# Performance work log

Measured on AMD Instinct MI355X. Metric: run time of the kernel, lower is better.

## Reference

```python
import jax, jax.numpy as jnp
import numpy as np

NUM_GRAPHS = 8
N_NODES = 50000
N_EDGES = 800000
F_IN = 128
HID = 256
EPS_BN = 1e-5


def _gat(x, ei, W, a_src, a_dst, b, heads, out_dim):
    # PyG GATConv: h = x @ W -> [N, heads, out]; edge (j=src -> i=dst)
    N = x.shape[0]
    h = (x @ W).reshape(N, heads, out_dim)
    alpha_src = jnp.sum(h * a_src, axis=-1)  # [N, H]
    alpha_dst = jnp.sum(h * a_dst, axis=-1)  # [N, H]
    src, dst = ei[0], ei[1]
    e = jax.nn.leaky_relu(alpha_src[src] + alpha_dst[dst], 0.2)  # [E, H]
    # segment softmax over edges grouped by destination node
    m = jax.ops.segment_max(e, dst, num_segments=N)
    m = jnp.where(jnp.isfinite(m), m, 0.0)
    ex = jnp.exp(e - m[dst])
    denom = jax.ops.segment_sum(ex, dst, num_segments=N)
    alpha = ex / (denom[dst] + 1e-16)
    msg = h[src] * alpha[:, :, None]  # [E, H, out]
    agg = jax.ops.segment_sum(msg, dst, num_segments=N)
    return agg.reshape(N, heads * out_dim) + b


def _bn(h, gamma, beta):
    # BatchNorm over nodes (training-mode batch statistics, biased variance)
    mu = h.mean(axis=0)
    var = h.var(axis=0)
    return gamma * (h - mu) / jnp.sqrt(var + EPS_BN) + beta


def setup_inputs() -> dict:
    key = jax.random.key(0)
    ks = jax.random.split(key, 16)
    s = 0.05
    inp = {
        "x": jax.random.normal(ks[0], (N_NODES, F_IN), dtype=jnp.float32),
        "edge_index": jax.random.randint(ks[1], (2, N_EDGES), 0, N_NODES, dtype=jnp.int64) if False else jax.random.randint(ks[1], (2, N_EDGES), 0, N_NODES),
        "batch_index": jnp.sort(jax.random.randint(ks[2], (N_NODES,), 0, NUM_GRAPHS)),
        # conv1: GATConv(128, 64, heads=4)
        "W1": jax.random.normal(ks[3], (F_IN, HID), dtype=jnp.float32) * s,
        "a_src1": jax.random.normal(ks[4], (4, 64), dtype=jnp.float32) * s,
        "a_dst1": jax.random.normal(ks[5], (4, 64), dtype=jnp.float32) * s,
        "b1": jnp.zeros((HID,), jnp.float32),
        "g1": jnp.ones((HID,), jnp.float32),
        "beta1": jnp.zeros((HID,), jnp.float32),
        # conv2: GATConv(256, 256, heads=1)
        "W2": jax.random.normal(ks[6], (HID, HID), dtype=jnp.float32) * s,
        "a_src2": jax.random.normal(ks[7], (1, HID), dtype=jnp.float32) * s,
        "a_dst2": jax.random.normal(ks[8], (1, HID), dtype=jnp.float32) * s,
        "b2": jnp.zeros((HID,), jnp.float32),
        "g2": jnp.ones((HID,), jnp.float32),
        "beta2": jnp.zeros((HID,), jnp.float32),
        # q_head: Linear(512,256) -> ReLU -> Linear(256,4)
        "Wq1": jax.random.normal(ks[9], (2 * HID, HID), dtype=jnp.float32) * s,
        "bq1": jnp.zeros((HID,), jnp.float32),
        "Wq2": jax.random.normal(ks[10], (HID, 4), dtype=jnp.float32) * s,
        "bq2": jnp.zeros((4,), jnp.float32),
    }
    return inp


def reference(x, edge_index, batch_index, W1, a_src1, a_dst1, b1, g1, beta1,
              W2, a_src2, a_dst2, b2, g2, beta2, Wq1, bq1, Wq2, bq2):
    N = x.shape[0]
    loops = jnp.arange(N, dtype=edge_index.dtype)
    ei = jnp.concatenate([edge_index, jnp.stack([loops, loops])], axis=1)
    h = jax.nn.relu(_bn(_gat(x, ei, W1, a_src1, a_dst1, b1, 4, 64), g1, beta1))
    h = jax.nn.relu(_bn(_gat(h, ei, W2, a_src2, a_dst2, b2, 1, HID), g2, beta2))
    sums = jax.ops.segment_sum(h, batch_index, num_segments=NUM_GRAPHS)
    cnt = jax.ops.segment_sum(jnp.ones((N, 1), h.dtype), batch_index, num_segments=NUM_GRAPHS)
    gmean = sums / jnp.maximum(cnt, 1.0)
    ctx = jnp.concatenate([h, gmean[batch_index]], axis=1)  # [N, 512]
    q = jax.nn.relu(ctx @ Wq1 + bq1) @ Wq2 + bq2  # [N, 4]
    return (q, batch_index)
```

## Files before the change

### kernel.cpp

```cpp
#include <hip/hip_runtime.h>
#include <hip/hip_bf16.h>
#include <math.h>

#define F_IN  128
#define HIDC  256
#define NG    8
#define EPS_BN 1e-5f

typedef unsigned short u16;
typedef unsigned int   u32;
typedef unsigned char  u8;
typedef __attribute__((ext_vector_type(8))) short bf16x8;
typedef __attribute__((ext_vector_type(4))) float f32x4;
typedef __attribute__((ext_vector_type(2))) float f32x2;

static __device__ __forceinline__ float b2f(u16 u) {
    return __uint_as_float((u32)u << 16);
}
static __device__ __forceinline__ u16 f2b(float f) {
    u32 u = __float_as_uint(f);
    u32 r = (u + 0x7fffu + ((u >> 16) & 1u)) >> 16;
    return (u16)r;
}
static __device__ __forceinline__ u32 pack2(float a, float b) {
    return (u32)f2b(a) | ((u32)f2b(b) << 16);
}
static __device__ __forceinline__ float lk(float v) {
    return v >= 0.f ? v : 0.2f * v;
}
static __device__ __forceinline__ u8 f2fp8(float v) {
    return (u8)__builtin_amdgcn_cvt_pk_fp8_f32(v, v, 0, false);
}

static __device__ __forceinline__ u16 frag_elem(const float* __restrict__ W,
                                                int i, int K) {
    int j = i & 7;
    int lane = (i >> 3) & 63;
    int rest = i >> 9;
    int ksteps = K >> 5;
    int kst = rest % ksteps;
    int ntile = rest / ksteps;
    int k = kst * 32 + (lane >> 4) * 8 + j;
    int n = ntile * 16 + (lane & 15);
    return f2b(W[(long)k * HIDC + n]);
}

__global__ void prep_kernel(const float* __restrict__ x,
                            const float* __restrict__ W1,
                            const float* __restrict__ W2,
                            const float* __restrict__ Wq1,
                            u32* __restrict__ xb, u16* __restrict__ WT1,
                            u16* __restrict__ WT2, u16* __restrict__ WQT,
                            int npair) {
    int i = blockIdx.x * 256 + threadIdx.x;
    if (i < npair) {
        float2 v = ((const float2*)x)[i];
        xb[i] = pack2(v.x, v.y);
        return;
    }
    i -= npair;
    if (i < F_IN * HIDC) { WT1[i] = frag_elem(W1, i, F_IN); return; }
    i -= F_IN * HIDC;
    if (i < HIDC * HIDC) { WT2[i] = frag_elem(W2, i, HIDC); return; }
    i -= HIDC * HIDC;
    if (i < HIDC * HIDC) { WQT[i] = frag_elem(Wq1, i, HIDC); }
}

__global__ void out_init_kernel(float* __restrict__ out,
                                const float* __restrict__ bq2,
                                const int* __restrict__ batch, int N) {
    int i = blockIdx.x * 256 + threadIdx.x;
    if (i < N * 4) out[i] = bq2[i & 3];
    else if (i < N * 5) out[i] = (float)batch[i - N * 4];
}

__global__ void bn_coef_kernel(const float* __restrict__ sum,
                               const float* __restrict__ sumsq,
                               const float* __restrict__ gamma,
                               const float* __restrict__ beta,
                               float* __restrict__ scale,
                               float* __restrict__ bias, int N) {
    int c = threadIdx.x;
    float invN = 1.f / (float)N;
    float mu = sum[c] * invN;
    float var = sumsq[c] * invN - mu * mu;
    float inv = rsqrtf(var + EPS_BN);
    float sc = gamma[c] * inv;
    scale[c] = sc;
    bias[c] = beta[c] - mu * sc;
}

template <int K, int MODE>
__global__ __launch_bounds__(256)
void gemm_mfma_kernel(const u16* __restrict__ A, const u16* __restrict__ WTf,
                      u8* __restrict__ C, int M,
                      const float* __restrict__ scaleA, const float* __restrict__ biasA,
                      const float* __restrict__ wsrc, const float* __restrict__ wdst,
                      float* __restrict__ asrc, float* __restrict__ adst,
                      const float* __restrict__ gproj, const int* __restrict__ bat,
                      const float* __restrict__ bq1,
                      const float* __restrict__ wq2, float* __restrict__ qout) {
    constexpr int KSTEPS = K / 32;
    constexpr int RCH = K / 8;
    __shared__ u16 sA[32][K + 8];
    int tid = threadIdx.x;
    int m0 = blockIdx.x * 32;

    for (int i = tid; i < 32 * RCH; i += 256) {
        int r = i / RCH, c = i % RCH;
        int gm = m0 + r;
        gm = gm < M ? gm : M - 1;
        *(uint4*)&sA[r][c * 8] = *(const uint4*)(A + (size_t)gm * K + c * 8);
    }
    __syncthreads();

    int wid = tid >> 6, lane = tid & 63;
    int row = lane & 15, quad = lane >> 4;
    int mf0 = m0, mf1 = m0 + 16;
    bool v1 = mf1 < M;

    f32x4 acc[2][4];
#pragma unroll
    for (int f = 0; f < 2; ++f)
#pragma unroll
        for (int t = 0; t < 4; ++t) acc[f][t] = (f32x4){0.f, 0.f, 0.f, 0.f};

    const u16* Bbase = WTf + ((size_t)(wid * 4) * KSTEPS * 64 + lane) * 8;

#pragma unroll
    for (int ks = 0; ks < KSTEPS; ++ks) {
        int kk = ks * 32 + quad * 8;
        bf16x8 a[2];
        a[0] = *(const bf16x8*)&sA[row][kk];
        a[1] = *(const bf16x8*)&sA[16 + row][kk];
        if constexpr (MODE != 0) {
            int c0 = kk;
            float4 s0 = *(const float4*)(scaleA + c0);
            float4 s1 = *(const float4*)(scaleA + c0 + 4);
            float4 b0 = *(const float4*)(biasA + c0);
            float4 b1 = *(const float4*)(biasA + c0 + 4);
#pragma unroll
            for (int f = 0; f < 2; ++f) {
                float xv[8];
#pragma unroll
                for (int j = 0; j < 8; ++j) xv[j] = b2f((u16)a[f][j]);
                xv[0] = fmaxf(fmaf(s0.x, xv[0], b0.x), 0.f);
                xv[1] = fmaxf(fmaf(s0.y, xv[1], b0.y), 0.f);
                xv[2] = fmaxf(fmaf(s0.z, xv[2], b0.z), 0.f);
                xv[3] = fmaxf(fmaf(s0.w, xv[3], b0.w), 0.f);
                xv[4] = fmaxf(fmaf(s1.x, xv[4], b1.x), 0.f);
                xv[5] = fmaxf(fmaf(s1.y, xv[5], b1.y), 0.f);
                xv[6] = fmaxf(fmaf(s1.z, xv[6], b1.z), 0.f);
                xv[7] = fmaxf(fmaf(s1.w, xv[7], b1.w), 0.f);
#pragma unroll
                for (int j = 0; j < 8; ++j) a[f][j] = (short)f2b(xv[j]);
            }
        }
#pragma unroll
        for (int t = 0; t < 4; ++t) {
            bf16x8 b = *(const bf16x8*)(Bbase + ((size_t)t * KSTEPS + ks) * 512);
            acc[0][t] = __builtin_amdgcn_mfma_f32_16x16x32_bf16(a[0], b, acc[0][t], 0, 0, 0);
            acc[1][t] = __builtin_amdgcn_mfma_f32_16x16x32_bf16(a[1], b, acc[1][t], 0, 0, 0);
        }
    }

    int n0 = wid * 64;
    int mf[2] = {mf0, mf1};
    bool vf[2] = {true, v1};
    if constexpr (MODE == 2) {
        float qacc[2][4][4];
#pragma unroll
        for (int f = 0; f < 2; ++f)
#pragma unroll
            for (int r = 0; r < 4; ++r)
#pragma unroll
                for (int j = 0; j < 4; ++j) qacc[f][r][j] = 0.f;
#pragma unroll
        for (int f = 0; f < 2; ++f) {
            if (!vf[f]) continue;
            int bm[4];
#pragma unroll
            for (int r = 0; r < 4; ++r) bm[r] = bat[mf[f] + quad * 4 + r];
#pragma unroll
            for (int t = 0; t < 4; ++t) {
                int n = n0 + t * 16 + row;
                float bq = bq1[n];
                float4 w4 = ((const float4*)wq2)[n];
#pragma unroll
                for (int r = 0; r < 4; ++r) {
                    float v = fmaxf(acc[f][t][r] + gproj[bm[r] * HIDC + n] + bq, 0.f);
                    qacc[f][r][0] = fmaf(v, w4.x, qacc[f][r][0]);
                    qacc[f][r][1] = fmaf(v, w4.y, qacc[f][r][1]);
                    qacc[f][r][2] = fmaf(v, w4.z, qacc[f][r][2]);
                    qacc[f][r][3] = fmaf(v, w4.w, qacc[f][r][3]);
                }
            }
        }
#pragma unroll
        for (int off = 1; off < 16; off <<= 1)
#pragma unroll
            for (int f = 0; f < 2; ++f)
#pragma unroll
                for (int r = 0; r < 4; ++r)
#pragma unroll
                    for (int j = 0; j < 4; ++j)
                        qacc[f][r][j] += __shfl_xor(qacc[f][r][j], off, 64);
        if (row == 0) {
#pragma unroll
            for (int f = 0; f < 2; ++f) {
                if (!vf[f]) continue;
#pragma unroll
                for (int r = 0; r < 4; ++r) {
                    size_t m = mf[f] + quad * 4 + r;
#pragma unroll
                    for (int j = 0; j < 4; ++j)
                        atomicAdd(&qout[m * 4 + j], qacc[f][r][j]);
                }
            }
        }
    } else {
#pragma unroll
        for (int f = 0; f < 2; ++f) {
            if (!vf[f]) continue;
#pragma unroll
            for (int t = 0; t < 4; ++t) {
                int n = n0 + t * 16 + row;
#pragma unroll
                for (int r = 0; r < 4; ++r)
                    C[(size_t)(mf[f] + quad * 4 + r) * HIDC + n] = f2fp8(acc[f][t][r]);
            }
        }
        if constexpr (MODE == 0) {
            float pa[2][4] = {}, pd[2][4] = {};
#pragma unroll
            for (int t = 0; t < 4; ++t) {
                float ws = wsrc[n0 + t * 16 + row];
                float wd = wdst[n0 + t * 16 + row];
#pragma unroll
                for (int f = 0; f < 2; ++f)
#pragma unroll
                    for (int r = 0; r < 4; ++r) {
                        pa[f][r] = fmaf(acc[f][t][r], ws, pa[f][r]);
                        pd[f][r] = fmaf(acc[f][t][r], wd, pd[f][r]);
                    }
            }
#pragma unroll
            for (int off = 1; off < 16; off <<= 1)
#pragma unroll
                for (int f = 0; f < 2; ++f)
#pragma unroll
                    for (int r = 0; r < 4; ++r) {
                        pa[f][r] += __shfl_xor(pa[f][r], off, 64);
                        pd[f][r] += __shfl_xor(pd[f][r], off, 64);
                    }
            if (row == 0) {
#pragma unroll
                for (int f = 0; f < 2; ++f) {
                    if (!vf[f]) continue;
#pragma unroll
                    for (int r = 0; r < 4; ++r) {
                        int m = mf[f] + quad * 4 + r;
                        asrc[m * 4 + wid] = pa[f][r];
                        adst[m * 4 + wid] = pd[f][r];
                    }
                }
            }
        }
        if constexpr (MODE == 1) {
            float pa[2][4] = {}, pd[2][4] = {};
#pragma unroll
            for (int t = 0; t < 4; ++t) {
                float ws = wsrc[n0 + t * 16 + row];
                float wd = wdst[n0 + t * 16 + row];
#pragma unroll
                for (int f = 0; f < 2; ++f)
#pragma unroll
                    for (int r = 0; r < 4; ++r) {
                        pa[f][r] = fmaf(acc[f][t][r], ws, pa[f][r]);
                        pd[f][r] = fmaf(acc[f][t][r], wd, pd[f][r]);
                    }
            }
#pragma unroll
            for (int off = 1; off < 16; off <<= 1)
#pragma unroll
                for (int f = 0; f < 2; ++f)
#pragma unroll
                    for (int r = 0; r < 4; ++r) {
                        pa[f][r] += __shfl_xor(pa[f][r], off, 64);
                        pd[f][r] += __shfl_xor(pd[f][r], off, 64);
                    }
            if (row == 0) {
#pragma unroll
                for (int f = 0; f < 2; ++f) {
                    if (!vf[f]) continue;
#pragma unroll
                    for (int r = 0; r < 4; ++r) {
                        int m = mf[f] + quad * 4 + r;
                        atomicAdd(&asrc[m], pa[f][r]);
                        atomicAdd(&adst[m], pd[f][r]);
                    }
                }
            }
        }
    }
}

__global__ void deg_kernel(const int* __restrict__ ei, int E, int N,
                           int* __restrict__ deg) {
    int e = blockIdx.x * blockDim.x + threadIdx.x;
    if (e >= E + N) return;
    int d = (e < E) ? ei[E + e] : (e - E);
    atomicAdd(&deg[d], 1);
}

__global__ __launch_bounds__(256)
void scan_phase1(const int* __restrict__ deg, int* __restrict__ part,
                 int* __restrict__ bsum, int N) {
    __shared__ int tmp[256];
    int i = blockIdx.x * 256 + threadIdx.x;
    int v = (i < N) ? deg[i] : 0;
    tmp[threadIdx.x] = v;
    __syncthreads();
    for (int off = 1; off < 256; off <<= 1) {
        int t = (threadIdx.x >= off) ? tmp[threadIdx.x - off] : 0;
        __syncthreads();
        tmp[threadIdx.x] += t;
        __syncthreads();
    }
    if (i < N) part[i] = tmp[threadIdx.x];
    if (threadIdx.x == 255) bsum[blockIdx.x] = tmp[255];
}
__global__ __launch_bounds__(256)
void scan_phase2(int* __restrict__ bsum, int nb) {
    __shared__ int tmp[256];
    int v = (threadIdx.x < nb) ? bsum[threadIdx.x] : 0;
    tmp[threadIdx.x] = v;
    __syncthreads();
    for (int off = 1; off < 256; off <<= 1) {
        int t = (threadIdx.x >= off) ? tmp[threadIdx.x - off] : 0;
        __syncthreads();
        tmp[threadIdx.x] += t;
        __syncthreads();
    }
    if (threadIdx.x < nb)
        bsum[threadIdx.x] = threadIdx.x ? tmp[threadIdx.x - 1] : 0;
}
__global__ __launch_bounds__(256)
void scan_phase3(const int* __restrict__ part, const int* __restrict__ bsum,
                 int* __restrict__ rowptr, int N) {
    int i = blockIdx.x * 256 + threadIdx.x;
    if (i < N) rowptr[i + 1] = part[i] + bsum[blockIdx.x];
    if (i == 0) rowptr[0] = 0;
}

__global__ void fill_kernel(const int* __restrict__ ei, int E, int N,
                            const int* __restrict__ rowptr,
                            int* __restrict__ cur, int* __restrict__ csr_src) {
    int e = blockIdx.x * blockDim.x + threadIdx.x;
    if (e >= E + N) return;
    int s = (e < E) ? ei[e] : (e - E);
    int d = (e < E) ? ei[E + e] : (e - E);
    int pos = rowptr[d] + atomicAdd(&cur[d], 1);
    csr_src[pos] = s;
}

template <int H>
__global__ __launch_bounds__(256)
void gat_gather_kernel(const int* __restrict__ rowptr,
                       const int* __restrict__ csr_src,
                       const float* __restrict__ asrc,
                       const float* __restrict__ adst,
                       const u8* __restrict__ h,
                       u16* __restrict__ agg, int N) {
    __shared__ __align__(16) uint2 s_ed[4][64 * H];
    int wid = threadIdx.x >> 6, lane = threadIdx.x & 63;
    int n = blockIdx.x * 4 + wid;
    if (n >= N) return;
    int start = rowptr[n], end = rowptr[n + 1];
    int deg = end - start;
    float ad[H];
#pragma unroll
    for (int hh = 0; hh < H; ++hh) ad[hh] = adst[n * H + hh];

    f32x2 acc01 = {0.f, 0.f}, acc23 = {0.f, 0.f};
    const int head = (H == 4) ? (lane >> 4) : 0;
    const u8* hb = h;
    const u32 laneB = (u32)lane * 4u;
    float wsum[H];

#define GBODY(J) {                                                             \
            uint2 e_ = s_ed[wid][(H == 4) ? ((J) * 4 + head) : (J)];           \
            u32 hv_ = *(const u32*)(hb + (size_t)(e_.x + laneB));              \
            float al_ = __uint_as_float(e_.y);                                 \
            f32x2 al2_ = {al_, al_};                                           \
            f32x2 v01_ = __builtin_amdgcn_cvt_pk_f32_fp8(hv_, false);          \
            f32x2 v23_ = __builtin_amdgcn_cvt_pk_f32_fp8(hv_, true);           \
            acc01 = __builtin_elementwise_fma(v01_, al2_, acc01);              \
            acc23 = __builtin_elementwise_fma(v23_, al2_, acc23); }

    if (deg <= 64) {
        float v[H];
#pragma unroll
        for (int hh = 0; hh < H; ++hh) v[hh] = -1e30f;
        u32 off = 0;
        if (lane < deg) {
            int s = csr_src[start + lane];
            off = (u32)s * (u32)HIDC;
            if (H == 4) {
                float4 a4 = *(const float4*)(asrc + s * 4);
                v[0] = lk(a4.x + ad[0]);
                v[1 % H] = lk(a4.y + ad[1 % H]);
                v[2 % H] = lk(a4.z + ad[2 % H]);
                v[3 % H] = lk(a4.w + ad[3 % H]);
            } else {
                v[0] = lk(asrc[s] + ad[0]);
            }
        }
        float m[H];
#pragma unroll
        for (int hh = 0; hh < H; ++hh) m[hh] = v[hh];
#pragma unroll
        for (int o = 1; o < 64; o <<= 1)
#pragma unroll
            for (int hh = 0; hh < H; ++hh)
                m[hh] = fmaxf(m[hh], __shfl_xor(m[hh], o, 64));
        float w[H];
#pragma unroll
        for (int hh = 0; hh < H; ++hh) {
            w[hh] = __expf(v[hh] - m[hh]);
            wsum[hh] = w[hh];
        }
#pragma unroll
        for (int o = 1; o < 64; o <<= 1)
#pragma unroll
            for (int hh = 0; hh < H; ++hh)
                wsum[hh] += __shfl_xor(wsum[hh], o, 64);
        if (H == 4) {
            uint4 w0, w1;
            w0.x = off; w0.y = __float_as_uint(w[0]);
            w0.z = off; w0.w = __float_as_uint(w[1 % H]);
            w1.x = off; w1.y = __float_as_uint(w[2 % H]);
            w1.z = off; w1.w = __float_as_uint(w[3 % H]);
            *(uint4*)&s_ed[wid][lane * 4] = w0;
            *(uint4*)&s_ed[wid][lane * 4 + 2] = w1;
        } else {
            s_ed[wid][lane] = make_uint2(off, __float_as_uint(w[0]));
        }
        int j = 0;
        for (; j + 4 <= deg; j += 4) { GBODY(j) GBODY(j + 1) GBODY(j + 2) GBODY(j + 3) }
        for (; j < deg; ++j) GBODY(j)
    } else {
        float m[H];
#pragma unroll
        for (int hh = 0; hh < H; ++hh) m[hh] = -1e30f;
        for (int i = start + lane; i < end; i += 64) {
            int s = csr_src[i];
            if (H == 4) {
                float4 a4 = *(const float4*)(asrc + s * 4);
                m[0] = fmaxf(m[0], lk(a4.x + ad[0]));
                m[1 % H] = fmaxf(m[1 % H], lk(a4.y + ad[1 % H]));
                m[2 % H] = fmaxf(m[2 % H], lk(a4.z + ad[2 % H]));
                m[3 % H] = fmaxf(m[3 % H], lk(a4.w + ad[3 % H]));
            } else {
                m[0] = fmaxf(m[0], lk(asrc[s] + ad[0]));
            }
        }
#pragma unroll
        for (int o = 1; o < 64; o <<= 1)
#pragma unroll
            for (int hh = 0; hh < H; ++hh)
                m[hh] = fmaxf(m[hh], __shfl_xor(m[hh], o, 64));
#pragma unroll
        for (int hh = 0; hh < H; ++hh) wsum[hh] = 0.f;
        for (int base = start; base < end; base += 64) {
            int cnt = min(64, end - base);
            if (lane < cnt) {
                int s = csr_src[base + lane];
                u32 off = (u32)s * (u32)HIDC;
                if (H == 4) {
                    float4 a4 = *(const float4*)(asrc + s * 4);
                    float w0f = __expf(lk(a4.x + ad[0]) - m[0]);
                    float w1f = __expf(lk(a4.y + ad[1 % H]) - m[1 % H]);
                    float w2f = __expf(lk(a4.z + ad[2 % H]) - m[2 % H]);
                    float w3f = __expf(lk(a4.w + ad[3 % H]) - m[3 % H]);
                    wsum[0] += w0f; wsum[1 % H] += w1f;
                    wsum[2 % H] += w2f; wsum[3 % H] += w3f;
                    uint4 w0, w1;
                    w0.x = off; w0.y = __float_as_uint(w0f);
                    w0.z = off; w0.w = __float_as_uint(w1f);
                    w1.x = off; w1.y = __float_as_uint(w2f);
                    w1.z = off; w1.w = __float_as_uint(w3f);
                    *(uint4*)&s_ed[wid][lane * 4] = w0;
                    *(uint4*)&s_ed[wid][lane * 4 + 2] = w1;
                } else {
                    float wf = __expf(lk(asrc[s] + ad[0]) - m[0]);
                    wsum[0] += wf;
                    s_ed[wid][lane] = make_uint2(off, __float_as_uint(wf));
                }
            }
            int j = 0;
            for (; j + 4 <= cnt; j += 4) { GBODY(j) GBODY(j + 1) GBODY(j + 2) GBODY(j + 3) }
            for (; j < cnt; ++j) GBODY(j)
        }
#pragma unroll
        for (int o = 1; o < 64; o <<= 1)
#pragma unroll
            for (int hh = 0; hh < H; ++hh)
                wsum[hh] += __shfl_xor(wsum[hh], o, 64);
    }
#undef GBODY
    float sc = 1.f / (wsum[head] + 1e-16f);
    f32x2 sc2 = {sc, sc};
    acc01 *= sc2;
    acc23 *= sc2;
    uint2 o;
    o.x = pack2(acc01.x, acc01.y);
    o.y = pack2(acc23.x, acc23.y);
    ((uint2*)(agg + (size_t)n * HIDC))[lane] = o;
}

__global__ __launch_bounds__(256)
void bn_stats_kernel(const u16* __restrict__ h, int N,
                     float* __restrict__ sum, float* __restrict__ sumsq) {
    int c = threadIdx.x;
    int r0 = blockIdx.x * 128;
    int rend = min(r0 + 128, N);
    float s = 0.f, q = 0.f;
    for (int r = r0; r < rend; ++r) {
        float v = b2f(h[(long)r * HIDC + c]);
        s += v;
        q += v * v;
    }
    atomicAdd(&sum[c], s);
    atomicAdd(&sumsq[c], q);
}

__global__ __launch_bounds__(256)
void pool_bn_kernel(const u16* __restrict__ h, const int* __restrict__ batch,
                    int N, const float* __restrict__ scale,
                    const float* __restrict__ bias,
                    float* __restrict__ gsum, float* __restrict__ gcnt) {
    int c = threadIdx.x;
    float sc = scale[c], bi = bias[c];
    int r0 = blockIdx.x * 128;
    int rend = min(r0 + 128, N);
    int curb = -1;
    float acc = 0.f;
    for (int r = r0; r < rend; ++r) {
        int b = batch[r];
        if (b != curb) {
            if (curb >= 0) atomicAdd(&gsum[curb * HIDC + c], acc);
            curb = b; acc = 0.f;
        }
        acc += fmaxf(fmaf(sc, b2f(h[(long)r * HIDC + c]), bi), 0.f);
    }
    if (curb >= 0) atomicAdd(&gsum[curb * HIDC + c], acc);
    if (c == 0) {
        int prev = -1; float cnt = 0.f;
        for (int r = r0; r < rend; ++r) {
            int b = batch[r];
            if (b != prev) {
                if (prev >= 0) atomicAdd(&gcnt[prev], cnt);
                prev = b; cnt = 0.f;
            }
            cnt += 1.f;
        }
        if (prev >= 0) atomicAdd(&gcnt[prev], cnt);
    }
}

__global__ __launch_bounds__(256)
void gmean_gproj_kernel(const float* __restrict__ gsum,
                        const float* __restrict__ gcnt,
                        const float* __restrict__ Wq1,
                        float* __restrict__ gproj) {
    int b = blockIdx.x, c = threadIdx.x;
    __shared__ float gm[HIDC];
    gm[c] = gsum[b * HIDC + c] / fmaxf(gcnt[b], 1.f);
    __syncthreads();
    float acc = 0.f;
    for (int k = 0; k < HIDC; ++k)
        acc = fmaf(gm[k], Wq1[(long)(HIDC + k) * HIDC + c], acc);
    gproj[b * HIDC + c] = acc;
}

extern "C" void kernel_launch(void* const* d_in, const int* in_sizes, int n_in,
                              void* d_out, int out_size, void* d_ws, size_t ws_size,
                              hipStream_t stream) {
    const float* x   = (const float*)d_in[0];
    const int*   ei  = (const int*)d_in[1];
    const int*   bat = (const int*)d_in[2];
    const float* W1  = (const float*)d_in[3];
    const float* as1 = (const float*)d_in[4];
    const float* ad1 = (const float*)d_in[5];
    const float* g1  = (const float*)d_in[7];
    const float* be1 = (const float*)d_in[8];
    const float* W2  = (const float*)d_in[9];
    const float* as2 = (const float*)d_in[10];
    const float* ad2 = (const float*)d_in[11];
    const float* g2  = (const float*)d_in[13];
    const float* be2 = (const float*)d_in[14];
    const float* Wq1 = (const float*)d_in[15];
    const float* bq1 = (const float*)d_in[16];
    const float* Wq2 = (const float*)d_in[17];
    const float* bq2 = (const float*)d_in[18];
    float* out = (float*)d_out;

    const int N = in_sizes[0] / F_IN;
    const int E = in_sizes[1] / 2;
    const int Etot = E + N;
    const int nb = (N + 255) / 256;

    const size_t hbytes = (size_t)N * HIDC * sizeof(u16);
    char* p = (char*)d_ws;
    auto alloc = [&](size_t sz) { char* q = p; p += (sz + 255) & ~(size_t)255; return q; };
    u16* BX   = (u16*)alloc((size_t)N * F_IN * sizeof(u16));
    u8*  BH   = (u8*)alloc((size_t)N * HIDC);
    u16* BA   = (u16*)alloc(hbytes);
    u16* WT1  = (u16*)alloc((size_t)HIDC * F_IN * sizeof(u16));
    u16* WT2  = (u16*)alloc((size_t)HIDC * HIDC * sizeof(u16));
    u16* WQT  = (u16*)alloc((size_t)HIDC * HIDC * sizeof(u16));
    float* asrc = (float*)alloc((size_t)N * 4 * 4 * 2);
    float* adst = asrc + (size_t)N * 4;
    int* rowptr  = (int*)alloc((size_t)(N + 1) * 4);
    int* csr_src = (int*)alloc((size_t)Etot * 4);
    int* cur     = (int*)alloc((size_t)N * 4 * 2);
    int* cur2    = cur + N;
    int* part    = (int*)alloc((size_t)N * 4);
    int* bsum    = (int*)alloc((size_t)nb * 4);
    float* bnsum = (float*)alloc(HIDC * 4 * 2);
    float* bnsq  = bnsum + HIDC;
    float* sc1   = (float*)alloc(HIDC * 4);
    float* bi1   = (float*)alloc(HIDC * 4);
    float* sc2   = (float*)alloc(HIDC * 4);
    float* bi2   = (float*)alloc(HIDC * 4);
    float* gsum  = (float*)alloc((NG * HIDC + NG) * 4);
    float* gcnt  = gsum + NG * HIDC;
    float* gproj = (float*)alloc(NG * HIDC * 4);

    dim3 gemmGrid((N + 31) / 32);
    int edgeBlocks = (Etot + 255) / 256;
    int nodeBlocksW = (N + 3) / 4;
    int npair = N * F_IN / 2;
    int prepTotal = npair + F_IN * HIDC + 2 * HIDC * HIDC;

    hipMemsetAsync(cur, 0, (size_t)N * 4 * 2, stream);
    deg_kernel<<<edgeBlocks, 256, 0, stream>>>(ei, E, N, cur);
    scan_phase1<<<nb, 256, 0, stream>>>(cur, part, bsum, N);
    scan_phase2<<<1, 256, 0, stream>>>(bsum, nb);
    scan_phase3<<<nb, 256, 0, stream>>>(part, bsum, rowptr, N);
    fill_kernel<<<edgeBlocks, 256, 0, stream>>>(ei, E, N, rowptr, cur2, csr_src);

    prep_kernel<<<(prepTotal + 255) / 256, 256, 0, stream>>>(
        x, W1, W2, Wq1, (u32*)BX, WT1, WT2, WQT, npair);

    gemm_mfma_kernel<F_IN, 0><<<gemmGrid, 256, 0, stream>>>(
        BX, WT1, BH, N, nullptr, nullptr, as1, ad1, asrc, adst,
        nullptr, nullptr, nullptr, nullptr, nullptr);
    gat_gather_kernel<4><<<nodeBlocksW, 256, 0, stream>>>(rowptr, csr_src, asrc, adst, BH, BA, N);
    hipMemsetAsync(bnsum, 0, HIDC * 4 * 2, stream);
    bn_stats_kernel<<<(N + 127) / 128, 256, 0, stream>>>(BA, N, bnsum, bnsq);
    bn_coef_kernel<<<1, HIDC, 0, stream>>>(bnsum, bnsq, g1, be1, sc1, bi1, N);

    hipMemsetAsync(asrc, 0, (size_t)N * 4 * 4 * 2, stream);
    gemm_mfma_kernel<HIDC, 1><<<gemmGrid, 256, 0, stream>>>(
        BA, WT2, BH, N, sc1, bi1, as2, ad2, asrc, adst,
        nullptr, nullptr, nullptr, nullptr, nullptr);
    gat_gather_kernel<1><<<nodeBlocksW, 256, 0, stream>>>(rowptr, csr_src, asrc, adst, BH, BA, N);
    hipMemsetAsync(bnsum, 0, HIDC * 4 * 2, stream);
    bn_stats_kernel<<<(N + 127) / 128, 256, 0, stream>>>(BA, N, bnsum, bnsq);
    bn_coef_kernel<<<1, HIDC, 0, stream>>>(bnsum, bnsq, g2, be2, sc2, bi2, N);

    hipMemsetAsync(gsum, 0, (NG * HIDC + NG) * 4, stream);
    pool_bn_kernel<<<(N + 127) / 128, 256, 0, stream>>>(BA, bat, N, sc2, bi2, gsum, gcnt);
    gmean_gproj_kernel<<<NG, HIDC, 0, stream>>>(gsum, gcnt, Wq1, gproj);
    out_init_kernel<<<(N * 5 + 255) / 256, 256, 0, stream>>>(out, bq2, bat, N);

    gemm_mfma_kernel<HIDC, 2><<<gemmGrid, 256, 0, stream>>>(
        BA, WQT, nullptr, N, sc2, bi2, nullptr, nullptr, nullptr, nullptr,
        gproj, bat, bq1, Wq2, out);
}
```

Measured before the change: 531.5 us.

## Fuse BN coefficient and output init into GEMMs, swap MFMA operands for row-wise epilogue

Removes the bn_coef and out_init kernels by computing BatchNorm scale/bias inside each GEMM block (into shared memory) and in the pool kernel, and by writing the batch-index tail from pool_bn. MFMA operands are swapped so each lane holds four consecutive columns of one row. This allows packed 4-byte fp8 stores, vectorized weight loads and cross-wave reductions through shared memory instead of global atomics for attention scores and q outputs. The asrc memset is also dropped. The cost is redundant per-block coefficient math and extra shared memory and barriers.

```diff
diff --git a/kernel.cpp b/kernel.cpp
--- a/kernel.cpp
+++ b/kernel.cpp
@@ -27,9 +27,6 @@
 }
 static __device__ __forceinline__ float lk(float v) {
     return v >= 0.f ? v : 0.2f * v;
-}
-static __device__ __forceinline__ u8 f2fp8(float v) {
-    return (u8)__builtin_amdgcn_cvt_pk_fp8_f32(v, v, 0, false);
 }
 
 static __device__ __forceinline__ u16 frag_elem(const float* __restrict__ W,
@@ -66,46 +63,36 @@
     if (i < HIDC * HIDC) { WQT[i] = frag_elem(Wq1, i, HIDC); }
 }
 
-__global__ void out_init_kernel(float* __restrict__ out,
-                                const float* __restrict__ bq2,
-                                const int* __restrict__ batch, int N) {
-    int i = blockIdx.x * 256 + threadIdx.x;
-    if (i < N * 4) out[i] = bq2[i & 3];
-    else if (i < N * 5) out[i] = (float)batch[i - N * 4];
-}
-
-__global__ void bn_coef_kernel(const float* __restrict__ sum,
-                               const float* __restrict__ sumsq,
-                               const float* __restrict__ gamma,
-                               const float* __restrict__ beta,
-                               float* __restrict__ scale,
-                               float* __restrict__ bias, int N) {
-    int c = threadIdx.x;
-    float invN = 1.f / (float)N;
-    float mu = sum[c] * invN;
-    float var = sumsq[c] * invN - mu * mu;
-    float inv = rsqrtf(var + EPS_BN);
-    float sc = gamma[c] * inv;
-    scale[c] = sc;
-    bias[c] = beta[c] - mu * sc;
-}
-
 template <int K, int MODE>
 __global__ __launch_bounds__(256)
 void gemm_mfma_kernel(const u16* __restrict__ A, const u16* __restrict__ WTf,
                       u8* __restrict__ C, int M,
-                      const float* __restrict__ scaleA, const float* __restrict__ biasA,
+                      const float* __restrict__ bnsum, const float* __restrict__ bnsq,
+                      const float* __restrict__ gamma, const float* __restrict__ beta,
                       const float* __restrict__ wsrc, const float* __restrict__ wdst,
                       float* __restrict__ asrc, float* __restrict__ adst,
                       const float* __restrict__ gproj, const int* __restrict__ bat,
                       const float* __restrict__ bq1,
-                      const float* __restrict__ wq2, float* __restrict__ qout) {
+                      const float* __restrict__ wq2, const float* __restrict__ bq2,
+                      float* __restrict__ qout) {
     constexpr int KSTEPS = K / 32;
     constexpr int RCH = K / 8;
     __shared__ u16 sA[32][K + 8];
+    __shared__ __align__(16) float sCoef[HIDC];
+    __shared__ __align__(16) float sBias[HIDC];
+    __shared__ __align__(16) float sExtra[512];
     int tid = threadIdx.x;
     int m0 = blockIdx.x * 32;
 
+    if constexpr (MODE != 0) {
+        float invN = 1.f / (float)M;
+        float mu = bnsum[tid] * invN;
+        float var = bnsq[tid] * invN - mu * mu;
+        float inv = rsqrtf(var + EPS_BN);
+        float sc = gamma[tid] * inv;
+        sCoef[tid] = sc;
+        sBias[tid] = beta[tid] - mu * sc;
+    }
     for (int i = tid; i < 32 * RCH; i += 256) {
         int r = i / RCH, c = i % RCH;
         int gm = m0 + r;
@@ -116,14 +103,14 @@
 
     int wid = tid >> 6, lane = tid & 63;
     int row = lane & 15, quad = lane >> 4;
-    int mf0 = m0, mf1 = m0 + 16;
-    bool v1 = mf1 < M;
+    bool v1 = (m0 + 16) < M;
+    int wave_n0 = wid * 64;
 
     f32x4 acc[2][4];
 #pragma unroll
-    for (int f = 0; f < 2; ++f)
-#pragma unroll
-        for (int t = 0; t < 4; ++t) acc[f][t] = (f32x4){0.f, 0.f, 0.f, 0.f};
+    for (int g = 0; g < 2; ++g)
+#pragma unroll
+        for (int t = 0; t < 4; ++t) acc[g][t] = (f32x4){0.f, 0.f, 0.f, 0.f};
 
     const u16* Bbase = WTf + ((size_t)(wid * 4) * KSTEPS * 64 + lane) * 8;
 
@@ -134,16 +121,15 @@
         a[0] = *(const bf16x8*)&sA[row][kk];
         a[1] = *(const bf16x8*)&sA[16 + row][kk];
         if constexpr (MODE != 0) {
-            int c0 = kk;
-            float4 s0 = *(const float4*)(scaleA + c0);
-            float4 s1 = *(const float4*)(scaleA + c0 + 4);
-            float4 b0 = *(const float4*)(biasA + c0);
-            float4 b1 = *(const float4*)(biasA + c0 + 4);
-#pragma unroll
-            for (int f = 0; f < 2; ++f) {
+            float4 s0 = *(const float4*)&sCoef[kk];
+            float4 s1 = *(const float4*)&sCoef[kk + 4];
+            float4 b0 = *(const float4*)&sBias[kk];
+            float4 b1 = *(const float4*)&sBias[kk + 4];
+#pragma unroll
+            for (int g = 0; g < 2; ++g) {
                 float xv[8];
 #pragma unroll
-                for (int j = 0; j < 8; ++j) xv[j] = b2f((u16)a[f][j]);
+                for (int j = 0; j < 8; ++j) xv[j] = b2f((u16)a[g][j]);
                 xv[0] = fmaxf(fmaf(s0.x, xv[0], b0.x), 0.f);
                 xv[1] = fmaxf(fmaf(s0.y, xv[1], b0.y), 0.f);
                 xv[2] = fmaxf(fmaf(s0.z, xv[2], b0.z), 0.f);
@@ -153,153 +139,141 @@
                 xv[6] = fmaxf(fmaf(s1.z, xv[6], b1.z), 0.f);
                 xv[7] = fmaxf(fmaf(s1.w, xv[7], b1.w), 0.f);
 #pragma unroll
-                for (int j = 0; j < 8; ++j) a[f][j] = (short)f2b(xv[j]);
+                for (int j = 0; j < 8; ++j) a[g][j] = (short)f2b(xv[j]);
             }
         }
 #pragma unroll
         for (int t = 0; t < 4; ++t) {
             bf16x8 b = *(const bf16x8*)(Bbase + ((size_t)t * KSTEPS + ks) * 512);
-            acc[0][t] = __builtin_amdgcn_mfma_f32_16x16x32_bf16(a[0], b, acc[0][t], 0, 0, 0);
-            acc[1][t] = __builtin_amdgcn_mfma_f32_16x16x32_bf16(a[1], b, acc[1][t], 0, 0, 0);
-        }
-    }
-
-    int n0 = wid * 64;
-    int mf[2] = {mf0, mf1};
+            acc[0][t] = __builtin_amdgcn_mfma_f32_16x16x32_bf16(b, a[0], acc[0][t], 0, 0, 0);
+            acc[1][t] = __builtin_amdgcn_mfma_f32_16x16x32_bf16(b, a[1], acc[1][t], 0, 0, 0);
+        }
+    }
+
     bool vf[2] = {true, v1};
     if constexpr (MODE == 2) {
-        float qacc[2][4][4];
-#pragma unroll
-        for (int f = 0; f < 2; ++f)
-#pragma unroll
-            for (int r = 0; r < 4; ++r)
-#pragma unroll
-                for (int j = 0; j < 4; ++j) qacc[f][r][j] = 0.f;
-#pragma unroll
-        for (int f = 0; f < 2; ++f) {
-            if (!vf[f]) continue;
-            int bm[4];
-#pragma unroll
-            for (int r = 0; r < 4; ++r) bm[r] = bat[mf[f] + quad * 4 + r];
+        float qa[2][4];
+#pragma unroll
+        for (int g = 0; g < 2; ++g)
+#pragma unroll
+            for (int j = 0; j < 4; ++j) qa[g][j] = 0.f;
+        int bm[2];
+#pragma unroll
+        for (int g = 0; g < 2; ++g) {
+            int m = m0 + g * 16 + row;
+            bm[g] = bat[m < M ? m : M - 1];
+        }
+#pragma unroll
+        for (int t = 0; t < 4; ++t) {
+            int nb = wave_n0 + t * 16 + quad * 4;
+            float4 bq4 = *(const float4*)&bq1[nb];
+            float4 w4[4];
+#pragma unroll
+            for (int r = 0; r < 4; ++r) w4[r] = ((const float4*)wq2)[nb + r];
+#pragma unroll
+            for (int g = 0; g < 2; ++g) {
+                float4 gp4 = *(const float4*)&gproj[bm[g] * HIDC + nb];
+                float gp[4] = {gp4.x, gp4.y, gp4.z, gp4.w};
+                float bqv[4] = {bq4.x, bq4.y, bq4.z, bq4.w};
+#pragma unroll
+                for (int r = 0; r < 4; ++r) {
+                    float v = fmaxf(acc[g][t][r] + gp[r] + bqv[r], 0.f);
+                    qa[g][0] = fmaf(v, w4[r].x, qa[g][0]);
+                    qa[g][1] = fmaf(v, w4[r].y, qa[g][1]);
+                    qa[g][2] = fmaf(v, w4[r].z, qa[g][2]);
+                    qa[g][3] = fmaf(v, w4[r].w, qa[g][3]);
+                }
+            }
+        }
+#pragma unroll
+        for (int off = 16; off < 64; off <<= 1)
+#pragma unroll
+            for (int g = 0; g < 2; ++g)
+#pragma unroll
+                for (int j = 0; j < 4; ++j)
+                    qa[g][j] += __shfl_xor(qa[g][j], off, 64);
+        if (quad == 0) {
+#pragma unroll
+            for (int g = 0; g < 2; ++g) {
+                float4 v4 = {qa[g][0], qa[g][1], qa[g][2], qa[g][3]};
+                *(float4*)&sExtra[((wid * 2 + g) * 16 + row) * 4] = v4;
+            }
+        }
+        __syncthreads();
+        if (tid < 128) {
+            int g = tid >> 6, mm = (tid >> 2) & 15, j = tid & 3;
+            float v = 0.f;
+#pragma unroll
+            for (int w = 0; w < 4; ++w)
+                v += sExtra[((w * 2 + g) * 16 + mm) * 4 + j];
+            int m = m0 + g * 16 + mm;
+            if (m < M) qout[(size_t)m * 4 + j] = v + bq2[j];
+        }
+    } else {
+#pragma unroll
+        for (int g = 0; g < 2; ++g) {
+            if (!vf[g]) continue;
+            int m = m0 + g * 16 + row;
 #pragma unroll
             for (int t = 0; t < 4; ++t) {
-                int n = n0 + t * 16 + row;
-                float bq = bq1[n];
-                float4 w4 = ((const float4*)wq2)[n];
-#pragma unroll
-                for (int r = 0; r < 4; ++r) {
-                    float v = fmaxf(acc[f][t][r] + gproj[bm[r] * HIDC + n] + bq, 0.f);
-                    qacc[f][r][0] = fmaf(v, w4.x, qacc[f][r][0]);
-                    qacc[f][r][1] = fmaf(v, w4.y, qacc[f][r][1]);
-                    qacc[f][r][2] = fmaf(v, w4.z, qacc[f][r][2]);
-                    qacc[f][r][3] = fmaf(v, w4.w, qacc[f][r][3]);
+                u32 pk = __builtin_amdgcn_cvt_pk_fp8_f32(acc[g][t][0], acc[g][t][1], 0, false);
+                pk = __builtin_amdgcn_cvt_pk_fp8_f32(acc[g][t][2], acc[g][t][3], pk, true);
+                *(u32*)&C[(size_t)m * HIDC + wave_n0 + t * 16 + quad * 4] = pk;
+            }
+        }
+        float pa[2] = {0.f, 0.f}, pd[2] = {0.f, 0.f};
+#pragma unroll
+        for (int t = 0; t < 4; ++t) {
+            int nb = wave_n0 + t * 16 + quad * 4;
+            float4 ws4 = *(const float4*)&wsrc[nb];
+            float4 wd4 = *(const float4*)&wdst[nb];
+#pragma unroll
+            for (int g = 0; g < 2; ++g) {
+                pa[g] = fmaf(acc[g][t][0], ws4.x, pa[g]);
+                pa[g] = fmaf(acc[g][t][1], ws4.y, pa[g]);
+                pa[g] = fmaf(acc[g][t][2], ws4.z, pa[g]);
+                pa[g] = fmaf(acc[g][t][3], ws4.w, pa[g]);
+                pd[g] = fmaf(acc[g][t][0], wd4.x, pd[g]);
+                pd[g] = fmaf(acc[g][t][1], wd4.y, pd[g]);
+                pd[g] = fmaf(acc[g][t][2], wd4.z, pd[g]);
+                pd[g] = fmaf(acc[g][t][3], wd4.w, pd[g]);
+            }
+        }
+#pragma unroll
+        for (int off = 16; off < 64; off <<= 1)
+#pragma unroll
+            for (int g = 0; g < 2; ++g) {
+                pa[g] += __shfl_xor(pa[g], off, 64);
+                pd[g] += __shfl_xor(pd[g], off, 64);
+            }
+        if constexpr (MODE == 0) {
+            if (quad == 0) {
+#pragma unroll
+                for (int g = 0; g < 2; ++g) {
+                    if (!vf[g]) continue;
+                    int m = m0 + g * 16 + row;
+                    asrc[m * 4 + wid] = pa[g];
+                    adst[m * 4 + wid] = pd[g];
                 }
             }
         }
-#pragma unroll
-        for (int off = 1; off < 16; off <<= 1)
-#pragma unroll
-            for (int f = 0; f < 2; ++f)
-#pragma unroll
-                for (int r = 0; r < 4; ++r)
-#pragma unroll
-                    for (int j = 0; j < 4; ++j)
-                        qacc[f][r][j] += __shfl_xor(qacc[f][r][j], off, 64);
-        if (row == 0) {
-#pragma unroll
-            for (int f = 0; f < 2; ++f) {
-                if (!vf[f]) continue;
-#pragma unroll
-                for (int r = 0; r < 4; ++r) {
-                    size_t m = mf[f] + quad * 4 + r;
-#pragma unroll
-                    for (int j = 0; j < 4; ++j)
-                        atomicAdd(&qout[m * 4 + j], qacc[f][r][j]);
+        if constexpr (MODE == 1) {
+            if (quad == 0) {
+#pragma unroll
+                for (int g = 0; g < 2; ++g) {
+                    sExtra[((wid * 2 + g) * 2 + 0) * 16 + row] = pa[g];
+                    sExtra[((wid * 2 + g) * 2 + 1) * 16 + row] = pd[g];
                 }
             }
-        }
-    } else {
-#pragma unroll
-        for (int f = 0; f < 2; ++f) {
-            if (!vf[f]) continue;
-#pragma unroll
-            for (int t = 0; t < 4; ++t) {
-                int n = n0 + t * 16 + row;
-#pragma unroll
-                for (int r = 0; r < 4; ++r)
-                    C[(size_t)(mf[f] + quad * 4 + r) * HIDC + n] = f2fp8(acc[f][t][r]);
-            }
-        }
-        if constexpr (MODE == 0) {
-            float pa[2][4] = {}, pd[2][4] = {};
-#pragma unroll
-            for (int t = 0; t < 4; ++t) {
-                float ws = wsrc[n0 + t * 16 + row];
-                float wd = wdst[n0 + t * 16 + row];
-#pragma unroll
-                for (int f = 0; f < 2; ++f)
-#pragma unroll
-                    for (int r = 0; r < 4; ++r) {
-                        pa[f][r] = fmaf(acc[f][t][r], ws, pa[f][r]);
-                        pd[f][r] = fmaf(acc[f][t][r], wd, pd[f][r]);
-                    }
-            }
-#pragma unroll
-            for (int off = 1; off < 16; off <<= 1)
-#pragma unroll
-                for (int f = 0; f < 2; ++f)
-#pragma unroll
-                    for (int r = 0; r < 4; ++r) {
-                        pa[f][r] += __shfl_xor(pa[f][r], off, 64);
-                        pd[f][r] += __shfl_xor(pd[f][r], off, 64);
-                    }
-            if (row == 0) {
-#pragma unroll
-                for (int f = 0; f < 2; ++f) {
-                    if (!vf[f]) continue;
-#pragma unroll
-                    for (int r = 0; r < 4; ++r) {
-                        int m = mf[f] + quad * 4 + r;
-                        asrc[m * 4 + wid] = pa[f][r];
-                        adst[m * 4 + wid] = pd[f][r];
-                    }
-                }
-            }
-        }
-        if constexpr (MODE == 1) {
-            float pa[2][4] = {}, pd[2][4] = {};
-#pragma unroll
-            for (int t = 0; t < 4; ++t) {
-                float ws = wsrc[n0 + t * 16 + row];
-                float wd = wdst[n0 + t * 16 + row];
-#pragma unroll
-                for (int f = 0; f < 2; ++f)
-#pragma unroll
-                    for (int r = 0; r < 4; ++r) {
-                        pa[f][r] = fmaf(acc[f][t][r], ws, pa[f][r]);
-                        pd[f][r] = fmaf(acc[f][t][r], wd, pd[f][r]);
-                    }
-            }
-#pragma unroll
-            for (int off = 1; off < 16; off <<= 1)
-#pragma unroll
-                for (int f = 0; f < 2; ++f)
-#pragma unroll
-                    for (int r = 0; r < 4; ++r) {
-                        pa[f][r] += __shfl_xor(pa[f][r], off, 64);
-                        pd[f][r] += __shfl_xor(pd[f][r], off, 64);
-                    }
-            if (row == 0) {
-#pragma unroll
-                for (int f = 0; f < 2; ++f) {
-                    if (!vf[f]) continue;
-#pragma unroll
-                    for (int r = 0; r < 4; ++r) {
-                        int m = mf[f] + quad * 4 + r;
-                        atomicAdd(&asrc[m], pa[f][r]);
-                        atomicAdd(&adst[m], pd[f][r]);
-                    }
-                }
+            __syncthreads();
+            if (tid < 64) {
+                int s = tid >> 5, g = (tid >> 4) & 1, mm = tid & 15;
+                float v = 0.f;
+#pragma unroll
+                for (int w = 0; w < 4; ++w)
+                    v += sExtra[((w * 2 + g) * 2 + s) * 16 + mm];
+                int m = m0 + g * 16 + mm;
+                if (m < M) (s == 0 ? asrc : adst)[m] = v;
             }
         }
     }
@@ -537,11 +511,19 @@
 
 __global__ __launch_bounds__(256)
 void pool_bn_kernel(const u16* __restrict__ h, const int* __restrict__ batch,
-                    int N, const float* __restrict__ scale,
-                    const float* __restrict__ bias,
-                    float* __restrict__ gsum, float* __restrict__ gcnt) {
+                    int N, const float* __restrict__ bnsum,
+                    const float* __restrict__ bnsq,
+                    const float* __restrict__ gamma,
+                    const float* __restrict__ beta,
+                    float* __restrict__ gsum, float* __restrict__ gcnt,
+                    float* __restrict__ outTail) {
     int c = threadIdx.x;
-    float sc = scale[c], bi = bias[c];
+    float invN = 1.f / (float)N;
+    float mu = bnsum[c] * invN;
+    float var = bnsq[c] * invN - mu * mu;
+    float inv = rsqrtf(var + EPS_BN);
+    float sc = gamma[c] * inv;
+    float bi = beta[c] - mu * sc;
     int r0 = blockIdx.x * 128;
     int rend = min(r0 + 128, N);
     int curb = -1;
@@ -555,6 +537,7 @@
         acc += fmaxf(fmaf(sc, b2f(h[(long)r * HIDC + c]), bi), 0.f);
     }
     if (curb >= 0) atomicAdd(&gsum[curb * HIDC + c], acc);
+    if (c < 128 && r0 + c < rend) outTail[r0 + c] = (float)batch[r0 + c];
     if (c == 0) {
         int prev = -1; float cnt = 0.f;
         for (int r = r0; r < rend; ++r) {
@@ -630,10 +613,6 @@
     int* bsum    = (int*)alloc((size_t)nb * 4);
     float* bnsum = (float*)alloc(HIDC * 4 * 2);
     float* bnsq  = bnsum + HIDC;
-    float* sc1   = (float*)alloc(HIDC * 4);
-    float* bi1   = (float*)alloc(HIDC * 4);
-    float* sc2   = (float*)alloc(HIDC * 4);
-    float* bi2   = (float*)alloc(HIDC * 4);
     float* gsum  = (float*)alloc((NG * HIDC + NG) * 4);
     float* gcnt  = gsum + NG * HIDC;
     float* gproj = (float*)alloc(NG * HIDC * 4);
@@ -655,28 +634,25 @@
         x, W1, W2, Wq1, (u32*)BX, WT1, WT2, WQT, npair);
 
     gemm_mfma_kernel<F_IN, 0><<<gemmGrid, 256, 0, stream>>>(
-        BX, WT1, BH, N, nullptr, nullptr, as1, ad1, asrc, adst,
-        nullptr, nullptr, nullptr, nullptr, nullptr);
+        BX, WT1, BH, N, nullptr, nullptr, nullptr, nullptr,
+        as1, ad1, asrc, adst, nullptr, nullptr, nullptr, nullptr, nullptr, nullptr);
     gat_gather_kernel<4><<<nodeBlocksW, 256, 0, stream>>>(rowptr, csr_src, asrc, adst, BH, BA, N);
     hipMemsetAsync(bnsum, 0, HIDC * 4 * 2, stream);
     bn_stats_kernel<<<(N + 127) / 128, 256, 0, stream>>>(BA, N, bnsum, bnsq);
-    bn_coef_kernel<<<1, HIDC, 0, stream>>>(bnsum, bnsq, g1, be1, sc1, bi1, N);
-
-    hipMemsetAsync(asrc, 0, (size_t)N * 4 * 4 * 2, stream);
+
     gemm_mfma_kernel<HIDC, 1><<<gemmGrid, 256, 0, stream>>>(
-        BA, WT2, BH, N, sc1, bi1, as2, ad2, asrc, adst,
-        nullptr, nullptr, nullptr, nullptr, nullptr);
+        BA, WT2, BH, N, bnsum, bnsq, g1, be1,
+        as2, ad2, asrc, adst, nullptr, nullptr, nullptr, nullptr, nullptr, nullptr);
     gat_gather_kernel<1><<<nodeBlocksW, 256, 0, stream>>>(rowptr, csr_src, asrc, adst, BH, BA, N);
     hipMemsetAsync(bnsum, 0, HIDC * 4 * 2, stream);
     bn_stats_kernel<<<(N + 127) / 128, 256, 0, stream>>>(BA, N, bnsum, bnsq);
-    bn_coef_kernel<<<1, HIDC, 0, stream>>>(bnsum, bnsq, g2, be2, sc2, bi2, N);
 
     hipMemsetAsync(gsum, 0, (NG * HIDC + NG) * 4, stream);
-    pool_bn_kernel<<<(N + 127) / 128, 256, 0, stream>>>(BA, bat, N, sc2, bi2, gsum, gcnt);
+    pool_bn_kernel<<<(N + 127) / 128, 256, 0, stream>>>(
+        BA, bat, N, bnsum, bnsq, g2, be2, gsum, gcnt, out + (size_t)N * 4);
     gmean_gproj_kernel<<<NG, HIDC, 0, stream>>>(gsum, gcnt, Wq1, gproj);
-    out_init_kernel<<<(N * 5 + 255) / 256, 256, 0, stream>>>(out, bq2, bat, N);
 
     gemm_mfma_kernel<HIDC, 2><<<gemmGrid, 256, 0, stream>>>(
-        BA, WQT, nullptr, N, sc2, bi2, nullptr, nullptr, nullptr, nullptr,
-        gproj, bat, bq1, Wq2, out);
-}
+        BA, WQT, nullptr, N, bnsum, bnsq, g2, be2,
+        nullptr, nullptr, nullptr, nullptr, gproj, bat, bq1, Wq2, bq2, out);
+}
```

Result: faster. 481.7 us (-9.4%).
